# Kernel optimization log

Measured on AMD Instinct MI355X. Metric: run time of the kernel, lower is better.

## Reference

```python
import jax, jax.numpy as jnp
import numpy as np

HEAD_NUM = 16


def setup_inputs() -> dict:
    key = jax.random.key(0)
    k1, k2, k3, k4 = jax.random.split(key, 4)
    B, S, E = 8, 1024, 1024
    inputs = jax.random.normal(k1, (B, S, E), dtype=jnp.float32)
    W_Query = jax.random.normal(k2, (E, E), dtype=jnp.float32) * 0.05
    W_Key = jax.random.normal(k3, (E, E), dtype=jnp.float32) * 0.05
    W_Value = jax.random.normal(k4, (E, E), dtype=jnp.float32) * 0.05
    return {"inputs": inputs, "W_Query": W_Query, "W_Key": W_Key, "W_Value": W_Value}


def reference(inputs, W_Query, W_Key, W_Value):
    B, S, E = inputs.shape
    H = HEAD_NUM
    D = E // H
    # QKV projections: [B,S,E] @ [E,E] -> [B,S,E]
    q = jnp.einsum('bse,ef->bsf', inputs, W_Query).reshape(B, S, H, D)
    k = jnp.einsum('bse,ef->bsf', inputs, W_Key).reshape(B, S, H, D)
    v = jnp.einsum('bse,ef->bsf', inputs, W_Value).reshape(B, S, H, D)
    # NOTE: original has NO 1/sqrt(D) scaling.
    scores = jnp.einsum('bihd,bjhd->bhij', q, k)  # [B,H,S,S]
    att = jax.nn.softmax(scores, axis=-1)
    out = jnp.einsum('bhij,bjhd->bihd', att, v).reshape(B, S, E)
    return jax.nn.relu(out)
```

## Files before the change

kernel.cpp:

```cpp
#include <hip/hip_runtime.h>
#include <cstdint>
#include <cstddef>

#define B_ 8
#define S_ 1024
#define E_ 1024
#define H_ 16
#define D_ 64
#define M_ (B_*S_)

typedef _Float16 f16;
typedef __attribute__((ext_vector_type(8))) _Float16 f16x8;
typedef __attribute__((ext_vector_type(4))) _Float16 f16x4;
typedef __attribute__((ext_vector_type(4))) float  f32x4;
typedef __attribute__((ext_vector_type(16))) float f32x16;
typedef __attribute__((ext_vector_type(4))) int    int4v;
typedef __attribute__((ext_vector_type(2))) int    int2v;

__device__ __forceinline__ f32x4 mfma16(f16x8 a, f16x8 b, f32x4 c) {
  return __builtin_amdgcn_mfma_f32_16x16x32_f16(a, b, c, 0, 0, 0);
}
__device__ __forceinline__ f32x16 mfma32(f16x8 a, f16x8 b, f32x16 c) {
  return __builtin_amdgcn_mfma_f32_32x32x16_f16(a, b, c, 0, 0, 0);
}
__device__ __forceinline__ void gll16(const f16* g, f16* l) {
  __builtin_amdgcn_global_load_lds(
      (const __attribute__((address_space(1))) void*)g,
      (__attribute__((address_space(3))) void*)l, 16, 0, 0);
}
__device__ __forceinline__ int pkrtz(float lo, float hi) {
  return __builtin_bit_cast(int, __builtin_amdgcn_cvt_pkrtz(lo, hi));
}

__global__ __launch_bounds__(256) void presplit_kernel(
    const float* __restrict__ X, f16* __restrict__ Xf) {
  size_t i = ((size_t)blockIdx.x * 256 + threadIdx.x) * 8;
  f32x4 v0 = *(const f32x4*)&X[i];
  f32x4 v1 = *(const f32x4*)&X[i + 4];
  f16x8 hv;
#pragma unroll
  for (int j = 0; j < 4; ++j) {
    hv[j] = (f16)v0[j];
    hv[j + 4] = (f16)v1[j];
  }
  *(f16x8*)&Xf[i] = hv;
}

__global__ __launch_bounds__(512) void wt_conv3_kernel(
    const float* __restrict__ Wq, const float* __restrict__ Wk,
    const float* __restrict__ Wv, f16* __restrict__ oq, f16* __restrict__ ok,
    f16* __restrict__ ov) {
  const float* W = blockIdx.z == 0 ? Wq : (blockIdx.z == 1 ? Wk : Wv);
  f16* o = blockIdx.z == 0 ? oq : (blockIdx.z == 1 ? ok : ov);
  const float scl = blockIdx.z == 0 ? 1.4426950408889634f : 1.0f;
  __shared__ float t[64][65];
  const int f0 = blockIdx.x * 64, e0 = blockIdx.y * 64;
  const int tx = threadIdx.x, ty = threadIdx.y;
#pragma unroll
  for (int j = 0; j < 8; ++j)
    t[ty + 8 * j][tx] = W[(size_t)(e0 + ty + 8 * j) * E_ + f0 + tx];
  __syncthreads();
#pragma unroll
  for (int j = 0; j < 8; ++j)
    o[(size_t)(f0 + ty + 8 * j) * E_ + e0 + tx] =
        (f16)(t[tx][ty + 8 * j] * scl);
}

__global__ __launch_bounds__(256) void gemm_qkv_kernel(
    const f16* __restrict__ Xf,
    const f16* __restrict__ Wq, const f16* __restrict__ Wk,
    const f16* __restrict__ Wv,
    f16* __restrict__ Qh, f16* __restrict__ Ql,
    f16* __restrict__ Kf, f16* __restrict__ Vt) {
  __shared__ f16 sA[128][64], sB[128][64];
  const int bid = blockIdx.x;
  const int xcd = bid & 7, idx = bid >> 3;
  const int mb = xcd * 8 + idx / 24;
  const int nb = idx % 24;
  const int z = nb >> 3;
  const int n0 = (nb & 7) * 128, m0 = mb * 128;
  const f16* __restrict__ Bt = z == 0 ? Wq : (z == 1 ? Wk : Wv);
  const int tid = threadIdx.x;
  const int lane = tid & 63, w = tid >> 6;
  const int wm = (w >> 1) * 64, wn = (w & 1) * 64;
  const int fr = lane & 15, fg = lane >> 4;
  f32x4 acc[4][4] = {};
  for (int k0 = 0; k0 < E_; k0 += 64) {
#pragma unroll
    for (int i = 0; i < 4; ++i) {
      int ci = tid + i * 256;
      int r = ci >> 3, cl = ci & 7;
      int cs = (cl ^ (r & 7)) * 8;
      gll16(Xf + (size_t)(m0 + r) * E_ + k0 + cs, &sA[0][0] + ci * 8);
      gll16(Bt + (size_t)(n0 + r) * E_ + k0 + cs, &sB[0][0] + ci * 8);
    }
    __syncthreads();
#pragma unroll
    for (int kh2 = 0; kh2 < 2; ++kh2) {
      f16x8 ah[4];
#pragma unroll
      for (int mi = 0; mi < 4; ++mi) {
        int rA = wm + mi * 16 + fr;
        ah[mi] = *(const f16x8*)&sA[rA][(((kh2 * 4 + fg) ^ (rA & 7))) * 8];
      }
#pragma unroll
      for (int ni = 0; ni < 4; ++ni) {
        int rB = wn + ni * 16 + fr;
        f16x8 bh = *(const f16x8*)&sB[rB][(((kh2 * 4 + fg) ^ (rB & 7))) * 8];
#pragma unroll
        for (int mi = 0; mi < 4; ++mi)
          acc[mi][ni] = mfma16(ah[mi], bh, acc[mi][ni]);
      }
    }
    __syncthreads();
  }
  if (z == 0) {
#pragma unroll
    for (int mi = 0; mi < 4; ++mi)
#pragma unroll
      for (int ni = 0; ni < 4; ++ni)
#pragma unroll
        for (int r = 0; r < 4; ++r) {
          int row = m0 + wm + mi * 16 + (lane >> 4) * 4 + r;
          int col = n0 + wn + ni * 16 + fr;
          float v = acc[mi][ni][r];
          int bb = row >> 10, s = row & 1023;
          int hd = col >> 6, d = col & 63;
          size_t idx2 = ((size_t)(bb * H_ + hd) * S_ + s) * D_ + d;
          f16 hh = (f16)v;
          Qh[idx2] = hh;
          Ql[idx2] = (f16)(v - (float)hh);
        }
  } else if (z == 1) {
#pragma unroll
    for (int mi = 0; mi < 4; ++mi)
#pragma unroll
      for (int ni = 0; ni < 4; ++ni)
#pragma unroll
        for (int r = 0; r < 4; ++r) {
          int row = m0 + wm + mi * 16 + (lane >> 4) * 4 + r;
          int col = n0 + wn + ni * 16 + fr;
          int bb = row >> 10, s = row & 1023;
          int hd = col >> 6, d = col & 63;
          Kf[((size_t)(bb * H_ + hd) * S_ + s) * D_ + d] = (f16)acc[mi][ni][r];
        }
  } else {
#pragma unroll
    for (int mi = 0; mi < 4; ++mi)
#pragma unroll
      for (int ni = 0; ni < 4; ++ni) {
        int row = m0 + wm + mi * 16 + (lane >> 4) * 4;
        int col = n0 + wn + ni * 16 + fr;
        int bb = row >> 10, s = row & 1023;
        int hd = col >> 6, d = col & 63;
        f16x4 p;
#pragma unroll
        for (int r = 0; r < 4; ++r) p[r] = (f16)acc[mi][ni][r];
        *(f16x4*)&Vt[((size_t)(bb * H_ + hd) * D_ + d) * S_ + s] = p;
      }
  }
}

__global__ __launch_bounds__(256, 3) void attn_kernel(
    const f16* __restrict__ Qh, const f16* __restrict__ Ql,
    const f16* __restrict__ Kf, const f16* __restrict__ Vt,
    float* __restrict__ out) {
  __shared__ f16 sK[3][64][64], sV[3][64][64];
  const int bid = blockIdx.x;
  const int bh = (bid & 7) * 16 + (bid >> 6);
  const int qb = (bid >> 3) & 7;
  const int hd = bh & 15, bb = bh >> 4;
  const int tid = threadIdx.x;
  const int lane = tid & 63, w = tid >> 6;
  const int cq = lane & 31, h = lane >> 5;
  const int rsw = cq & 7;
  const size_t base = (size_t)bh * (S_ * D_);
  const f16* Qh_p = Qh + base;
  const f16* Ql_p = Ql + base;
  const f16* Kf_p = Kf + base;
  const f16* Vt_p = Vt + base;
  const int q0 = qb * 128 + w * 32;

  f16x8 qh_[4], ql_[4];
#pragma unroll
  for (int ks = 0; ks < 4; ++ks) {
    size_t off = (size_t)(q0 + cq) * D_ + ks * 16 + 8 * h;
    qh_[ks] = *(const f16x8*)&Qh_p[off];
    ql_[ks] = *(const f16x8*)&Ql_p[off];
  }

  float m_run, l_run;
  f32x16 O[2] = {};
  f16x8 pf[4];

#define STAGE(buf, kb)                                                        \
  {                                                                           \
    _Pragma("unroll")                                                         \
    for (int half = 0; half < 2; ++half) {                                    \
      int ci = tid + half * 256;                                              \
      int row = ci >> 3, cl = ci & 7;                                         \
      int cs = cl ^ (row & 7);                                                \
      gll16(Kf_p + (size_t)((kb) + row) * D_ + cs * 8, &sK[buf][0][0] + ci * 8); \
      gll16(Vt_p + (size_t)row * S_ + (kb) + cs * 8, &sV[buf][0][0] + ci * 8);   \
    }                                                                         \
  }

#define QKT(scv, bufi)                                                        \
  {                                                                           \
    _Pragma("unroll")                                                         \
    for (int f = 0; f < 2; ++f) {                                             \
      _Pragma("unroll")                                                       \
      for (int ks = 0; ks < 4; ++ks) {                                        \
        int cc = ((2 * ks + h) ^ rsw) * 8;                                    \
        f16x8 kv = *(const f16x8*)&sK[bufi][f * 32 + cq][cc];                 \
        scv[f] = mfma32(kv, qh_[ks], scv[f]);                                 \
        scv[f] = mfma32(kv, ql_[ks], scv[f]);                                 \
      }                                                                       \
    }                                                                         \
  }

#define PVT(bufi)                                                             \
  {                                                                           \
    _Pragma("unroll")                                                         \
    for (int ks = 0; ks < 4; ++ks) {                                          \
      _Pragma("unroll")                                                       \
      for (int df = 0; df < 2; ++df) {                                        \
        int cc = ((2 * ks + h) ^ rsw) * 8;                                    \
        f16x8 vf = *(const f16x8*)&sV[bufi][df * 32 + cq][cc];                \
        O[df] = mfma32(vf, pf[ks], O[df]);                                    \
      }                                                                       \
    }                                                                         \
  }

#define PFBUILD(scv)                                                          \
  {                                                                           \
    _Pragma("unroll")                                                         \
    for (int f = 0; f < 2; ++f) {                                             \
      _Pragma("unroll")                                                       \
      for (int ksl = 0; ksl < 2; ++ksl) {                                     \
        int b0 = 8 * ksl;                                                     \
        int a1 = pkrtz(scv[f][b0 + 0], scv[f][b0 + 1]);                       \
        int b1 = pkrtz(scv[f][b0 + 4], scv[f][b0 + 5]);                       \
        int2v r1 = __builtin_amdgcn_permlane32_swap(a1, b1, false, false);    \
        int a2 = pkrtz(scv[f][b0 + 2], scv[f][b0 + 3]);                       \
        int b2 = pkrtz(scv[f][b0 + 6], scv[f][b0 + 7]);                       \
        int2v r2 = __builtin_amdgcn_permlane32_swap(a2, b2, false, false);    \
        int4v wd;                                                             \
        wd[0] = r1[0]; wd[1] = r2[0]; wd[2] = r1[1]; wd[3] = r2[1];           \
        pf[2 * f + ksl] = __builtin_bit_cast(f16x8, wd);                      \
      }                                                                       \
    }                                                                         \
  }

#define MAXTREE(pm, scv)                                                      \
  {                                                                           \
    float t4[4];                                                              \
    _Pragma("unroll")                                                         \
    for (int i = 0; i < 4; ++i) {                                             \
      float a = fmaxf(fmaxf(scv[0][i], scv[0][i + 4]),                        \
                      fmaxf(scv[0][i + 8], scv[0][i + 12]));                  \
      float b = fmaxf(fmaxf(scv[1][i], scv[1][i + 4]),                        \
                      fmaxf(scv[1][i + 8], scv[1][i + 12]));                  \
      t4[i] = fmaxf(a, b);                                                    \
    }                                                                         \
    pm = fmaxf(fmaxf(t4[0], t4[1]), fmaxf(t4[2], t4[3]));                     \
    pm = fmaxf(pm, __shfl_xor(pm, 32));                                       \
  }

#define ROWSUM(rs, scv)                                                       \
  {                                                                           \
    float rs0 = 0.f, rs1 = 0.f, rs2 = 0.f, rs3 = 0.f;                         \
    _Pragma("unroll")                                                         \
    for (int f = 0; f < 2; ++f) {                                             \
      _Pragma("unroll")                                                       \
      for (int r4 = 0; r4 < 4; ++r4) {                                        \
        rs0 += scv[f][4 * r4 + 0];                                            \
        rs1 += scv[f][4 * r4 + 1];                                            \
        rs2 += scv[f][4 * r4 + 2];                                            \
        rs3 += scv[f][4 * r4 + 3];                                            \
      }                                                                       \
    }                                                                         \
    rs = (rs0 + rs1) + (rs2 + rs3);                                           \
    rs += __shfl_xor(rs, 32);                                                 \
  }

  int bc = 0, bn = 1, bs = 2;
  STAGE(0, 0);
  asm volatile("s_waitcnt vmcnt(0)" ::: "memory");
  __builtin_amdgcn_sched_barrier(0);
  __builtin_amdgcn_s_barrier();
  STAGE(1, 64);
  {
    f32x16 sc[2] = {};
    QKT(sc, 0);
    float pm;
    MAXTREE(pm, sc);
    m_run = pm;
#pragma unroll
    for (int f = 0; f < 2; ++f)
#pragma unroll
      for (int r = 0; r < 16; ++r)
        sc[f][r] = __builtin_amdgcn_exp2f(sc[f][r] - pm);
    float rs;
    ROWSUM(rs, sc);
    l_run = rs;
    PFBUILD(sc);
  }

  for (int t = 0; t < 15; ++t) {
    asm volatile("s_waitcnt vmcnt(0)" ::: "memory");
    __builtin_amdgcn_sched_barrier(0);
    __builtin_amdgcn_s_barrier();

    f32x16 sc[2];
#pragma unroll
    for (int f = 0; f < 2; ++f)
#pragma unroll
      for (int r = 0; r < 16; ++r) sc[f][r] = -m_run;
    __builtin_amdgcn_s_setprio(1);
    QKT(sc, bn);
    __builtin_amdgcn_s_setprio(0);
    if (t < 14) STAGE(bs, (t + 2) * 64);

#pragma unroll
    for (int f = 0; f < 2; ++f)
#pragma unroll
      for (int r = 0; r < 16; ++r)
        sc[f][r] = __builtin_amdgcn_exp2f(sc[f][r]);
    float pm;
    MAXTREE(pm, sc);
    bool trig = __any(pm > 2048.f);
    float scl = 1.f;
    if (trig) {
      float pmx = fmaxf(pm, 1.0f);
      scl = 1.0f / pmx;
      m_run += __builtin_amdgcn_logf(pmx);
#pragma unroll
      for (int f = 0; f < 2; ++f)
#pragma unroll
        for (int r = 0; r < 16; ++r) sc[f][r] *= scl;
    }

    __builtin_amdgcn_s_setprio(1);
    PVT(bc);
    __builtin_amdgcn_s_setprio(0);

    if (trig) {
      l_run *= scl;
#pragma unroll
      for (int df = 0; df < 2; ++df)
#pragma unroll
        for (int i = 0; i < 16; ++i) O[df][i] *= scl;
    }
    float rs;
    ROWSUM(rs, sc);
    l_run += rs;
    PFBUILD(sc);
    int tmp = bc; bc = bn; bn = bs; bs = tmp;
  }
  PVT(bc);

  float inv = 1.0f / l_run;
  int s = q0 + cq;
  float* orow = out + ((size_t)bb * S_ + s) * E_ + hd * 64;
#pragma unroll
  for (int df = 0; df < 2; ++df)
#pragma unroll
    for (int g = 0; g < 4; ++g) {
      f32x4 vv;
#pragma unroll
      for (int j = 0; j < 4; ++j)
        vv[j] = fmaxf(O[df][4 * g + j] * inv, 0.f);
      *(f32x4*)&orow[df * 32 + 8 * g + 4 * h] = vv;
    }
}

extern "C" void kernel_launch(void* const* d_in, const int* in_sizes, int n_in,
                              void* d_out, int out_size, void* d_ws, size_t ws_size,
                              hipStream_t stream) {
  const float* X  = (const float*)d_in[0];
  const float* Wq = (const float*)d_in[1];
  const float* Wk = (const float*)d_in[2];
  const float* Wv = (const float*)d_in[3];
  float* out = (float*)d_out;
  char* ws = (char*)d_ws;

  const size_t WSZ = (size_t)E_ * E_ * sizeof(f16);
  const size_t QSZ = (size_t)M_ * E_ * sizeof(f16);
  f16* Wqf = (f16*)(ws);
  f16* Wkf = (f16*)(ws + WSZ);
  f16* Wvf = (f16*)(ws + 2 * WSZ);
  char* p = ws + 3 * WSZ;
  f16* Xf = (f16*)(p);
  f16* Qh = (f16*)(p + QSZ);
  f16* Ql = (f16*)(p + 2 * QSZ);
  f16* Kf = (f16*)(p + 3 * QSZ);
  f16* Vt = (f16*)(p + 4 * QSZ);

  presplit_kernel<<<4096, 256, 0, stream>>>(X, Xf);
  wt_conv3_kernel<<<dim3(16, 16, 3), dim3(64, 8), 0, stream>>>(
      Wq, Wk, Wv, Wqf, Wkf, Wvf);

  gemm_qkv_kernel<<<1536, 256, 0, stream>>>(
      Xf, Wqf, Wkf, Wvf, Qh, Ql, Kf, Vt);

  attn_kernel<<<1024, 256, 0, stream>>>(Qh, Ql, Kf, Vt, out);
}
```

Baseline: 147.0 us.

## Drop Q hi/lo split, compute row sums via MFMA, double-buffer attention

Q is now stored as a single f16 tensor instead of a high/low pair, which halves the QK^T MFMA count and removes one Q write and read. The softmax row sum is accumulated with an extra MFMA against a ones vector instead of VALU adds and a shuffle. The attention pipeline moves from a three-buffer to a two-buffer LDS ring, with launch bounds raised to 4 blocks per CU. The risk is lower score precision, since scores are unscaled and large, so exp2 of logits with f16-rounded Q may break accuracy tolerance.

```diff
diff --git a/kernel.cpp b/kernel.cpp
--- a/kernel.cpp
+++ b/kernel.cpp
@@ -70,8 +70,7 @@
     const f16* __restrict__ Xf,
     const f16* __restrict__ Wq, const f16* __restrict__ Wk,
     const f16* __restrict__ Wv,
-    f16* __restrict__ Qh, f16* __restrict__ Ql,
-    f16* __restrict__ Kf, f16* __restrict__ Vt) {
+    f16* __restrict__ Qf, f16* __restrict__ Kf, f16* __restrict__ Vt) {
   __shared__ f16 sA[128][64], sB[128][64];
   const int bid = blockIdx.x;
   const int xcd = bid & 7, idx = bid >> 3;
@@ -114,24 +113,8 @@
     }
     __syncthreads();
   }
-  if (z == 0) {
-#pragma unroll
-    for (int mi = 0; mi < 4; ++mi)
-#pragma unroll
-      for (int ni = 0; ni < 4; ++ni)
-#pragma unroll
-        for (int r = 0; r < 4; ++r) {
-          int row = m0 + wm + mi * 16 + (lane >> 4) * 4 + r;
-          int col = n0 + wn + ni * 16 + fr;
-          float v = acc[mi][ni][r];
-          int bb = row >> 10, s = row & 1023;
-          int hd = col >> 6, d = col & 63;
-          size_t idx2 = ((size_t)(bb * H_ + hd) * S_ + s) * D_ + d;
-          f16 hh = (f16)v;
-          Qh[idx2] = hh;
-          Ql[idx2] = (f16)(v - (float)hh);
-        }
-  } else if (z == 1) {
+  if (z < 2) {
+    f16* Of = z == 0 ? Qf : Kf;
 #pragma unroll
     for (int mi = 0; mi < 4; ++mi)
 #pragma unroll
@@ -142,7 +125,7 @@
           int col = n0 + wn + ni * 16 + fr;
           int bb = row >> 10, s = row & 1023;
           int hd = col >> 6, d = col & 63;
-          Kf[((size_t)(bb * H_ + hd) * S_ + s) * D_ + d] = (f16)acc[mi][ni][r];
+          Of[((size_t)(bb * H_ + hd) * S_ + s) * D_ + d] = (f16)acc[mi][ni][r];
         }
   } else {
 #pragma unroll
@@ -161,11 +144,10 @@
   }
 }
 
-__global__ __launch_bounds__(256, 3) void attn_kernel(
-    const f16* __restrict__ Qh, const f16* __restrict__ Ql,
-    const f16* __restrict__ Kf, const f16* __restrict__ Vt,
-    float* __restrict__ out) {
-  __shared__ f16 sK[3][64][64], sV[3][64][64];
+__global__ __launch_bounds__(256, 4) void attn_kernel(
+    const f16* __restrict__ Qf, const f16* __restrict__ Kf,
+    const f16* __restrict__ Vt, float* __restrict__ out) {
+  __shared__ f16 sK[2][64][64], sV[2][64][64];
   const int bid = blockIdx.x;
   const int bh = (bid & 7) * 16 + (bid >> 6);
   const int qb = (bid >> 3) & 7;
@@ -175,22 +157,22 @@
   const int cq = lane & 31, h = lane >> 5;
   const int rsw = cq & 7;
   const size_t base = (size_t)bh * (S_ * D_);
-  const f16* Qh_p = Qh + base;
-  const f16* Ql_p = Ql + base;
+  const f16* Qf_p = Qf + base;
   const f16* Kf_p = Kf + base;
   const f16* Vt_p = Vt + base;
   const int q0 = qb * 128 + w * 32;
 
-  f16x8 qh_[4], ql_[4];
-#pragma unroll
-  for (int ks = 0; ks < 4; ++ks) {
-    size_t off = (size_t)(q0 + cq) * D_ + ks * 16 + 8 * h;
-    qh_[ks] = *(const f16x8*)&Qh_p[off];
-    ql_[ks] = *(const f16x8*)&Ql_p[off];
-  }
-
-  float m_run, l_run;
-  f32x16 O[2] = {};
+  f16x8 qh_[4];
+#pragma unroll
+  for (int ks = 0; ks < 4; ++ks)
+    qh_[ks] = *(const f16x8*)&Qf_p[(size_t)(q0 + cq) * D_ + ks * 16 + 8 * h];
+
+  f16x8 ones;
+#pragma unroll
+  for (int j = 0; j < 8; ++j) ones[j] = (f16)1.0f;
+
+  float m_run;
+  f32x16 O[2] = {}, Ol = {};
   f16x8 pf[4];
 
 #define STAGE(buf, kb)                                                        \
@@ -214,22 +196,23 @@
         int cc = ((2 * ks + h) ^ rsw) * 8;                                    \
         f16x8 kv = *(const f16x8*)&sK[bufi][f * 32 + cq][cc];                 \
         scv[f] = mfma32(kv, qh_[ks], scv[f]);                                 \
-        scv[f] = mfma32(kv, ql_[ks], scv[f]);                                 \
       }                                                                       \
     }                                                                         \
   }
 
-#define PVT(bufi)                                                             \
-  {                                                                           \
-    _Pragma("unroll")                                                         \
-    for (int ks = 0; ks < 4; ++ks) {                                          \
-      _Pragma("unroll")                                                       \
-      for (int df = 0; df < 2; ++df) {                                        \
-        int cc = ((2 * ks + h) ^ rsw) * 8;                                    \
-        f16x8 vf = *(const f16x8*)&sV[bufi][df * 32 + cq][cc];                \
-        O[df] = mfma32(vf, pf[ks], O[df]);                                    \
-      }                                                                       \
-    }                                                                         \
+#define MAXTREE(pm, scv)                                                      \
+  {                                                                           \
+    float t4[4];                                                              \
+    _Pragma("unroll")                                                         \
+    for (int i = 0; i < 4; ++i) {                                             \
+      float a = fmaxf(fmaxf(scv[0][i], scv[0][i + 4]),                        \
+                      fmaxf(scv[0][i + 8], scv[0][i + 12]));                  \
+      float b = fmaxf(fmaxf(scv[1][i], scv[1][i + 4]),                        \
+                      fmaxf(scv[1][i + 8], scv[1][i + 12]));                  \
+      t4[i] = fmaxf(a, b);                                                    \
+    }                                                                         \
+    pm = fmaxf(fmaxf(t4[0], t4[1]), fmaxf(t4[2], t4[3]));                     \
+    pm = fmaxf(pm, __shfl_xor(pm, 32));                                       \
   }
 
 #define PFBUILD(scv)                                                          \
@@ -252,39 +235,20 @@
     }                                                                         \
   }
 
-#define MAXTREE(pm, scv)                                                      \
-  {                                                                           \
-    float t4[4];                                                              \
-    _Pragma("unroll")                                                         \
-    for (int i = 0; i < 4; ++i) {                                             \
-      float a = fmaxf(fmaxf(scv[0][i], scv[0][i + 4]),                        \
-                      fmaxf(scv[0][i + 8], scv[0][i + 12]));                  \
-      float b = fmaxf(fmaxf(scv[1][i], scv[1][i + 4]),                        \
-                      fmaxf(scv[1][i + 8], scv[1][i + 12]));                  \
-      t4[i] = fmaxf(a, b);                                                    \
-    }                                                                         \
-    pm = fmaxf(fmaxf(t4[0], t4[1]), fmaxf(t4[2], t4[3]));                     \
-    pm = fmaxf(pm, __shfl_xor(pm, 32));                                       \
-  }
-
-#define ROWSUM(rs, scv)                                                       \
-  {                                                                           \
-    float rs0 = 0.f, rs1 = 0.f, rs2 = 0.f, rs3 = 0.f;                         \
-    _Pragma("unroll")                                                         \
-    for (int f = 0; f < 2; ++f) {                                             \
+#define PVT(bufi)                                                             \
+  {                                                                           \
+    _Pragma("unroll")                                                         \
+    for (int ks = 0; ks < 4; ++ks) {                                          \
+      int cc = ((2 * ks + h) ^ rsw) * 8;                                      \
       _Pragma("unroll")                                                       \
-      for (int r4 = 0; r4 < 4; ++r4) {                                        \
-        rs0 += scv[f][4 * r4 + 0];                                            \
-        rs1 += scv[f][4 * r4 + 1];                                            \
-        rs2 += scv[f][4 * r4 + 2];                                            \
-        rs3 += scv[f][4 * r4 + 3];                                            \
+      for (int df = 0; df < 2; ++df) {                                        \
+        f16x8 vf = *(const f16x8*)&sV[bufi][df * 32 + cq][cc];                \
+        O[df] = mfma32(vf, pf[ks], O[df]);                                    \
       }                                                                       \
-    }                                                                         \
-    rs = (rs0 + rs1) + (rs2 + rs3);                                           \
-    rs += __shfl_xor(rs, 32);                                                 \
-  }
-
-  int bc = 0, bn = 1, bs = 2;
+      Ol = mfma32(ones, pf[ks], Ol);                                          \
+    }                                                                         \
+  }
+
   STAGE(0, 0);
   asm volatile("s_waitcnt vmcnt(0)" ::: "memory");
   __builtin_amdgcn_sched_barrier(0);
@@ -292,7 +256,9 @@
   STAGE(1, 64);
   {
     f32x16 sc[2] = {};
+    __builtin_amdgcn_s_setprio(1);
     QKT(sc, 0);
+    __builtin_amdgcn_s_setprio(0);
     float pm;
     MAXTREE(pm, sc);
     m_run = pm;
@@ -301,66 +267,63 @@
 #pragma unroll
       for (int r = 0; r < 16; ++r)
         sc[f][r] = __builtin_amdgcn_exp2f(sc[f][r] - pm);
-    float rs;
-    ROWSUM(rs, sc);
-    l_run = rs;
     PFBUILD(sc);
-  }
-
-  for (int t = 0; t < 15; ++t) {
+    __builtin_amdgcn_s_setprio(1);
+    PVT(0);
+    __builtin_amdgcn_s_setprio(0);
+  }
+  asm volatile("s_waitcnt vmcnt(0)" ::: "memory");
+  __builtin_amdgcn_sched_barrier(0);
+  __builtin_amdgcn_s_barrier();
+
+  for (int t = 1; t < 16; ++t) {
+    const int cur = t & 1;
+    if (t < 15) STAGE(cur ^ 1, (t + 1) * 64);
+
+    f32x16 sc[2];
+#pragma unroll
+    for (int f = 0; f < 2; ++f)
+#pragma unroll
+      for (int r = 0; r < 16; ++r) sc[f][r] = -m_run;
+    __builtin_amdgcn_s_setprio(1);
+    QKT(sc, cur);
+    __builtin_amdgcn_s_setprio(0);
+
+#pragma unroll
+    for (int f = 0; f < 2; ++f)
+#pragma unroll
+      for (int r = 0; r < 16; ++r)
+        sc[f][r] = __builtin_amdgcn_exp2f(sc[f][r]);
+
+    float pm;
+    MAXTREE(pm, sc);
+    if (__any(pm > 2048.f)) {
+      float pmx = fmaxf(pm, 1.0f);
+      float scl = 1.0f / pmx;
+      m_run += __builtin_amdgcn_logf(pmx);
+#pragma unroll
+      for (int f = 0; f < 2; ++f)
+#pragma unroll
+        for (int r = 0; r < 16; ++r) sc[f][r] *= scl;
+#pragma unroll
+      for (int df = 0; df < 2; ++df)
+#pragma unroll
+        for (int i = 0; i < 16; ++i) O[df][i] *= scl;
+#pragma unroll
+      for (int i = 0; i < 16; ++i) Ol[i] *= scl;
+    }
+
+    PFBUILD(sc);
+    __builtin_amdgcn_s_setprio(1);
+    PVT(cur);
+    __builtin_amdgcn_s_setprio(0);
+
     asm volatile("s_waitcnt vmcnt(0)" ::: "memory");
     __builtin_amdgcn_sched_barrier(0);
     __builtin_amdgcn_s_barrier();
-
-    f32x16 sc[2];
-#pragma unroll
-    for (int f = 0; f < 2; ++f)
-#pragma unroll
-      for (int r = 0; r < 16; ++r) sc[f][r] = -m_run;
-    __builtin_amdgcn_s_setprio(1);
-    QKT(sc, bn);
-    __builtin_amdgcn_s_setprio(0);
-    if (t < 14) STAGE(bs, (t + 2) * 64);
-
-#pragma unroll
-    for (int f = 0; f < 2; ++f)
-#pragma unroll
-      for (int r = 0; r < 16; ++r)
-        sc[f][r] = __builtin_amdgcn_exp2f(sc[f][r]);
-    float pm;
-    MAXTREE(pm, sc);
-    bool trig = __any(pm > 2048.f);
-    float scl = 1.f;
-    if (trig) {
-      float pmx = fmaxf(pm, 1.0f);
-      scl = 1.0f / pmx;
-      m_run += __builtin_amdgcn_logf(pmx);
-#pragma unroll
-      for (int f = 0; f < 2; ++f)
-#pragma unroll
-        for (int r = 0; r < 16; ++r) sc[f][r] *= scl;
-    }
-
-    __builtin_amdgcn_s_setprio(1);
-    PVT(bc);
-    __builtin_amdgcn_s_setprio(0);
-
-    if (trig) {
-      l_run *= scl;
-#pragma unroll
-      for (int df = 0; df < 2; ++df)
-#pragma unroll
-        for (int i = 0; i < 16; ++i) O[df][i] *= scl;
-    }
-    float rs;
-    ROWSUM(rs, sc);
-    l_run += rs;
-    PFBUILD(sc);
-    int tmp = bc; bc = bn; bn = bs; bs = tmp;
-  }
-  PVT(bc);
-
-  float inv = 1.0f / l_run;
+  }
+
+  float inv = 1.0f / Ol[0];
   int s = q0 + cq;
   float* orow = out + ((size_t)bb * S_ + s) * E_ + hd * 64;
 #pragma unroll
@@ -392,17 +355,16 @@
   f16* Wvf = (f16*)(ws + 2 * WSZ);
   char* p = ws + 3 * WSZ;
   f16* Xf = (f16*)(p);
-  f16* Qh = (f16*)(p + QSZ);
-  f16* Ql = (f16*)(p + 2 * QSZ);
-  f16* Kf = (f16*)(p + 3 * QSZ);
-  f16* Vt = (f16*)(p + 4 * QSZ);
+  f16* Qf = (f16*)(p + QSZ);
+  f16* Kf = (f16*)(p + 2 * QSZ);
+  f16* Vt = (f16*)(p + 3 * QSZ);
 
   presplit_kernel<<<4096, 256, 0, stream>>>(X, Xf);
   wt_conv3_kernel<<<dim3(16, 16, 3), dim3(64, 8), 0, stream>>>(
       Wq, Wk, Wv, Wqf, Wkf, Wvf);
 
   gemm_qkv_kernel<<<1536, 256, 0, stream>>>(
-      Xf, Wqf, Wkf, Wvf, Qh, Ql, Kf, Vt);
-
-  attn_kernel<<<1024, 256, 0, stream>>>(Qh, Ql, Kf, Vt, out);
-}
+      Xf, Wqf, Wkf, Wvf, Qf, Kf, Vt);
+
+  attn_kernel<<<1024, 256, 0, stream>>>(Qf, Kf, Vt, out);
+}
```

New measurement: 132.7 us. 9.7% less time.
